# Kernel optimization log

Measured on AMD Instinct MI355X. Metric: run time of the kernel, lower is better.

Reference implementation:

```python
import jax, jax.numpy as jnp
import numpy as np

NUM_HEADS = 12
HEAD_SIZE = 64
HIDDEN = NUM_HEADS * HEAD_SIZE  # 768
ONE_SIDED_WINDOW = 256          # attention_window 512 // 2
NEG = -10000.0


def setup_inputs() -> dict:
    key = jax.random.key(0)
    ks = jax.random.split(key, 16)
    B, W, E, H = 1, 2048, 128, HIDDEN
    std = 0.02
    def lin(kw, kb):
        return (jax.random.normal(kw, (H, H), jnp.float32) * std,
                jax.random.normal(kb, (H,), jnp.float32) * std)
    q_w, q_b = lin(ks[0], ks[1])
    k_w, k_b = lin(ks[2], ks[3])
    v_w, v_b = lin(ks[4], ks[5])
    w2e_w, w2e_b = lin(ks[6], ks[7])
    e2w_w, e2w_b = lin(ks[8], ks[9])
    e2e_w, e2e_b = lin(ks[10], ks[11])
    return {
        "word_hidden_states": jax.random.normal(ks[12], (B, W, H), jnp.float32),
        "entity_hidden_states": jax.random.normal(ks[13], (B, E, H), jnp.float32),
        "attention_mask": jnp.zeros((B, 1, 1, W + E), jnp.float32),
        "q_w": q_w, "q_b": q_b, "k_w": k_w, "k_b": k_b, "v_w": v_w, "v_b": v_b,
        "w2e_w": w2e_w, "w2e_b": w2e_b, "e2w_w": e2w_w, "e2w_b": e2w_b,
        "e2e_w": e2e_w, "e2e_b": e2e_b,
    }


def reference(word_hidden_states, entity_hidden_states, attention_mask,
              q_w, q_b, k_w, k_b, v_w, v_b,
              w2e_w, w2e_b, e2w_w, e2w_b, e2e_w, e2e_b):
    B, W, H = word_hidden_states.shape
    E = entity_hidden_states.shape[1]
    S = W + E

    def heads(x):  # [B, L, H] -> [B, nh, L, hd]
        return x.reshape(B, -1, NUM_HEADS, HEAD_SIZE).transpose(0, 2, 1, 3)

    concat = jnp.concatenate([word_hidden_states, entity_hidden_states], axis=1)
    k = heads(concat @ k_w + k_b)          # [B, nh, S, hd]
    v = heads(concat @ v_w + v_b)
    q_w2w = heads(word_hidden_states @ q_w + q_b)
    q_w2e = heads(word_hidden_states @ w2e_w + w2e_b)
    q_e2w = heads(entity_hidden_states @ e2w_w + e2w_b)
    q_e2e = heads(entity_hidden_states @ e2e_w + e2e_b)

    k_word, k_ent = k[:, :, :W], k[:, :, W:]

    # --- w2w: Longformer sliding-window QK^T, then _conversion to a dense
    # [B, nh, W, W] matrix with out-of-band entries set to -10000. ---
    w2w = jnp.einsum('bhid,bhjd->bhij', q_w2w, k_word)  # [B, nh, W, W]
    idx = jnp.arange(W)
    in_band = jnp.abs(idx[:, None] - idx[None, :]) <= ONE_SIDED_WINDOW  # [W, W]
    # diagonal mask: float_mask[j] (-10000 where attention_mask != 0) added
    # within the band (broadcast over heads / query positions)
    mask_words = attention_mask[:, 0, 0, :W]                # [B, W]
    float_mask = jnp.where(mask_words != 0.0, NEG, 0.0)     # [B, W]
    w2w = w2w + float_mask[:, None, None, :]
    # _conversion: out-of-band -> -10000; also exact zeros -> -10000 (source quirk)
    w2w = jnp.where(in_band[None, None] & (w2w != 0.0), w2w, NEG)

    # --- entity-aware dense blocks ---
    w2e = jnp.einsum('bhid,bhjd->bhij', q_w2e, k_ent)    # [B, nh, W, E]
    e2w = jnp.einsum('bhid,bhjd->bhij', q_e2w, k_word)   # [B, nh, E, W]
    e2e = jnp.einsum('bhid,bhjd->bhij', q_e2e, k_ent)    # [B, nh, E, E]

    word_scores = jnp.concatenate([w2w, w2e], axis=3)    # [B, nh, W, S]
    ent_scores = jnp.concatenate([e2w, e2e], axis=3)     # [B, nh, E, S]
    scores = jnp.concatenate([word_scores, ent_scores], axis=2)  # [B, nh, S, S]

    scores = scores / jnp.sqrt(jnp.float32(HEAD_SIZE)) + attention_mask
    probs = jax.nn.softmax(scores, axis=-1)

    ctx = jnp.einsum('bhij,bhjd->bhid', probs, v)        # [B, nh, S, hd]
    ctx = ctx.transpose(0, 2, 1, 3).reshape(B, S, H)
    return ctx[:, :W, :], ctx[:, W:, :]
```

## Files before the change

### kernel.cpp

```cpp
#include <hip/hip_runtime.h>

typedef __bf16 bf16x8 __attribute__((ext_vector_type(8)));
typedef unsigned short u16x8 __attribute__((ext_vector_type(8)));
typedef u16x8 u16x8_a __attribute__((may_alias));
typedef unsigned int u32x2 __attribute__((ext_vector_type(2)));
typedef u32x2 u32x2_a __attribute__((may_alias));
typedef unsigned int u32x4 __attribute__((ext_vector_type(4)));
typedef u32x4 u32x4_a __attribute__((may_alias));
typedef float f32x4 __attribute__((ext_vector_type(4)));

#define LOG2E 1.4426950408889634f
#define NEGV  -10000.0f

__device__ __forceinline__ unsigned int cvtpk(float lo, float hi){
  unsigned int r;
  asm("v_cvt_pk_bf16_f32 %0, %1, %2" : "=v"(r) : "v"(lo), "v"(hi));
  return r;
}
__device__ __forceinline__ bf16x8 ldb(const unsigned short* p){
  return __builtin_bit_cast(bf16x8, *(const u16x8_a*)p);
}
__device__ __forceinline__ void gload16(const unsigned short* g, unsigned short* l){
  __builtin_amdgcn_global_load_lds(
    (const __attribute__((address_space(1))) void*)g,
    (__attribute__((address_space(3))) void*)l, 16, 0, 0);
}

__global__ __launch_bounds__(256) void prep(
    const float* __restrict__ w0, const float* __restrict__ w1,
    const float* __restrict__ w2, const float* __restrict__ w3,
    const float* __restrict__ w4, const float* __restrict__ w5,
    const float* __restrict__ word, const float* __restrict__ ent,
    const float* __restrict__ am,
    unsigned short* __restrict__ outT, unsigned short* __restrict__ Abf,
    float* __restrict__ amT, float* __restrict__ negT)
{
  int z = blockIdx.z, tid = threadIdx.x;
  if (z == 6){
    size_t id = (size_t)blockIdx.y*24 + blockIdx.x;
    size_t e = (id*256 + tid)*8;
    const size_t WE = (size_t)2048*768;
    const float* s = (e < WE) ? (word + e) : (ent + (e - WE));
    float4 a = *(const float4*)s;
    float4 b = *(const float4*)(s+4);
    u32x4 v = {cvtpk(a.x,a.y), cvtpk(a.z,a.w), cvtpk(b.x,b.y), cvtpk(b.z,b.w)};
    *(u32x4_a*)(Abf + e) = v;
    return;
  }
  if (z == 7){
    if (blockIdx.y != 0 || blockIdx.x >= 9) return;
    int j = blockIdx.x*256 + tid;
    if (j < 2176){
      float a = am[j];
      amT[j]  = a * LOG2E;
      negT[j] = (a != 0.f) ? NEGV : 0.f;
    }
    return;
  }
  if (blockIdx.y >= 24) return;
  const float* src;
  switch (z){
    case 0: src = w0; break; case 1: src = w1; break; case 2: src = w2; break;
    case 3: src = w3; break; case 4: src = w4; break; default: src = w5; break;
  }
  unsigned short* dst = outT + (size_t)z * 589824;
  __shared__ float tile[32][33];
  int tx = tid & 31, ty = tid >> 5;
  int x0 = blockIdx.x*32, y0 = blockIdx.y*32;
  #pragma unroll
  for (int i=0;i<32;i+=8) tile[ty+i][tx] = src[(size_t)(y0+ty+i)*768 + x0+tx];
  __syncthreads();
  #pragma unroll
  for (int i=0;i<32;i+=16){
    unsigned int u = cvtpk(tile[tx][ty+i], tile[tx][ty+i+8]);
    dst[(size_t)(x0+ty+i)*768 + y0+tx]   = (unsigned short)u;
    dst[(size_t)(x0+ty+i+8)*768 + y0+tx] = (unsigned short)(u>>16);
  }
}

__global__ __launch_bounds__(256) void gemm_proj(
    const unsigned short* __restrict__ Abf,
    const unsigned short* __restrict__ wT,
    const float* __restrict__ bK, const float* __restrict__ bV,
    const float* __restrict__ bQ, const float* __restrict__ bWE,
    const float* __restrict__ bEW, const float* __restrict__ bEE,
    unsigned short* __restrict__ oK, unsigned short* __restrict__ VbT,
    unsigned short* __restrict__ oQ, unsigned short* __restrict__ oWE,
    unsigned short* __restrict__ oEW, unsigned short* __restrict__ oEE)
{
  int mt = blockIdx.x, ntile = blockIdx.y;
  int g, mg;
  if      (mt < 17){ g=0; mg=mt;    }
  else if (mt < 34){ g=1; mg=mt-17; }
  else if (mt < 50){ g=2; mg=mt-34; }
  else if (mt < 66){ g=3; mg=mt-50; }
  else if (mt < 67){ g=4; mg=0;     }
  else             { g=5; mg=0;     }
  int m0 = mg*128;
  const unsigned short* A = Abf + (size_t)((g>=4 ? 2048 : 0) + m0)*768;
  const unsigned short* B = wT + (size_t)g*589824;
  const float* bias; unsigned short* out;
  switch (g){
    case 0: bias=bK;  out=oK;  break;
    case 1: bias=bV;  out=0;   break;
    case 2: bias=bQ;  out=oQ;  break;
    case 3: bias=bWE; out=oWE; break;
    case 4: bias=bEW; out=oEW; break;
    default:bias=bEE; out=oEE; break;
  }
  int n0 = ntile*128;

  __shared__ __align__(16) unsigned short a_s[128*32];
  __shared__ __align__(16) unsigned short b_s[128*32];

  int tid  = threadIdx.x;
  int w    = tid>>6, lane = tid&63, quad = lane>>4, lr = lane&15;
  int wm   = (w&1)*64, wn = (w>>1)*64;

  f32x4 acc[4][4];
  #pragma unroll
  for (int i=0;i<4;i++) for (int j=0;j<4;j++) for (int r=0;r<4;r++) acc[i][j][r]=0.f;

  int srow = lane>>2;
  int scol = (lane&3)*8;
  const unsigned short* gA0 = A + (size_t)(w*32 + srow)*768 + scol;
  const unsigned short* gA1 = gA0 + (size_t)16*768;
  const unsigned short* gB0 = B + (size_t)(n0 + w*32 + srow)*768 + scol;
  const unsigned short* gB1 = gB0 + (size_t)16*768;
  unsigned short* lA0 = a_s + w*32*32;
  unsigned short* lA1 = lA0 + 16*32;
  unsigned short* lB0 = b_s + w*32*32;
  unsigned short* lB1 = lB0 + 16*32;

  for (int k0=0; k0<768; k0+=32){
    __syncthreads();
    gload16(gA0 + k0, lA0);
    gload16(gA1 + k0, lA1);
    gload16(gB0 + k0, lB0);
    gload16(gB1 + k0, lB1);
    __syncthreads();
    bf16x8 af[4], bfr[4];
    #pragma unroll
    for (int i=0;i<4;i++) af[i]  = ldb(a_s + (wm+i*16+lr)*32 + quad*8);
    #pragma unroll
    for (int j=0;j<4;j++) bfr[j] = ldb(b_s + (wn+j*16+lr)*32 + quad*8);
    #pragma unroll
    for (int i=0;i<4;i++)
      #pragma unroll
      for (int j=0;j<4;j++)
        acc[i][j] = __builtin_amdgcn_mfma_f32_16x16x32_bf16(af[i], bfr[j], acc[i][j], 0,0,0);
  }
  if (g == 1){
    #pragma unroll
    for (int j=0;j<4;j++){
      int col = n0 + wn + j*16 + lr;
      float bb = bias[col];
      #pragma unroll
      for (int i=0;i<4;i++){
        int rowb = m0 + wm + i*16 + quad*4;
        u32x2 uv = {cvtpk(acc[i][j][0]+bb, acc[i][j][1]+bb),
                    cvtpk(acc[i][j][2]+bb, acc[i][j][3]+bb)};
        *(u32x2_a*)(VbT + (size_t)col*2176 + rowb) = uv;
      }
    }
  } else {
    out += (size_t)m0*768;
    #pragma unroll
    for (int j=0;j<4;j++){
      int col = n0 + wn + j*16 + lr;
      float bb = bias[col];
      #pragma unroll
      for (int i=0;i<4;i++){
        int rowb = wm + i*16 + quad*4;
        unsigned int u01 = cvtpk(acc[i][j][0]+bb, acc[i][j][1]+bb);
        unsigned int u23 = cvtpk(acc[i][j][2]+bb, acc[i][j][3]+bb);
        out[(size_t)(rowb+0)*768 + col] = (unsigned short)u01;
        out[(size_t)(rowb+1)*768 + col] = (unsigned short)(u01>>16);
        out[(size_t)(rowb+2)*768 + col] = (unsigned short)u23;
        out[(size_t)(rowb+3)*768 + col] = (unsigned short)(u23>>16);
      }
    }
  }
}

__global__ __launch_bounds__(256) void attn_split(
  const unsigned short* __restrict__ Kb,  const unsigned short* __restrict__ VbT,
  const unsigned short* __restrict__ Qw,  const unsigned short* __restrict__ Qwe,
  const unsigned short* __restrict__ Qew, const unsigned short* __restrict__ Qee,
  const float* __restrict__ amT, const float* __restrict__ negT,
  float* __restrict__ outw, float* __restrict__ pO, float* __restrict__ pML)
{
  int lin = blockIdx.x + 80*blockIdx.y;
  int wid = (lin & 7)*120 + (lin >> 3);
  int bx = wid % 80;
  int h  = wid / 80;

  int tid = threadIdx.x, w = tid>>6, lane = tid&63, quad = lane>>4, lr = lane&15;
  bool isword = bx < 64;
  int qrb, kh, nsplit, eg=0, ehalf=0;
  const unsigned short *Qa, *Qb;
  if (isword){ qrb = bx*32 + (w>>1)*16; kh = w&1; nsplit = 2; Qa=Qw;  Qb=Qwe; }
  else       { int e = bx-64; eg = e>>1; ehalf = e&1;
               qrb = eg*16;             kh = w;   nsplit = 4; Qa=Qew; Qb=Qee; }
  int hofs = h*64;

  __shared__ __align__(16) unsigned int shb[4*64*21];
  unsigned int* p32w = shb + w*(16*44);

  const unsigned short* qr = Qa + (size_t)(qrb+lr)*768 + hofs + quad*8;
  bf16x8 qa0 = ldb(qr), qa1 = ldb(qr + 32);
  qr = Qb + (size_t)(qrb+lr)*768 + hofs + quad*8;
  bf16x8 qb0 = ldb(qr), qb1 = ldb(qr + 32);

  u16x8 onesu;
  #pragma unroll
  for (int i=0;i<8;i++) onesu[i] = 0x3F80;
  bf16x8 onesf = __builtin_bit_cast(bf16x8, onesu);

  float m = -1e30f;
  f32x4 o[4], l4;
  #pragma unroll
  for (int r=0;r<4;r++) l4[r] = 0.f;
  #pragma unroll
  for (int n2=0;n2<4;n2++) for (int r=0;r<4;r++) o[n2][r] = 0.f;

  int lo, nw, start, end, step;
  if (isword){
    lo = qrb - 256; if (lo < 0) lo = 0; lo &= ~31;
    int hi = qrb + 272; if (hi > 2048) hi = 2048; hi = (hi + 31) & ~31;
    nw = (hi - lo) >> 5;
    start = kh; end = nw + 4; step = 2;
  } else {
    lo = 0; nw = 64;
    start = ehalf*34 + kh; end = ehalf*34 + 34; step = 4;
  }
  int iq = qrb + lr;

  for (int c = start; c < end; c += 2*step){
    int c2r = c + step;
    bool ph = (c2r >= end);
    int c2 = ph ? c : c2r;

    bool entp1 = c  >= nw;  int j1 = entp1 ? (2048 + (c -nw)*32) : (lo + c *32);
    bool entp2 = c2 >= nw;  int j2 = entp2 ? (2048 + (c2-nw)*32) : (lo + c2*32);

    const unsigned short* kp1 = Kb + (size_t)(j1+lr)*768 + hofs + quad*8;
    bf16x8 kA0 = ldb(kp1),          kA1 = ldb(kp1 + 32);
    bf16x8 kA2 = ldb(kp1 + 16*768), kA3 = ldb(kp1 + 16*768 + 32);
    const unsigned short* kp2 = Kb + (size_t)(j2+lr)*768 + hofs + quad*8;
    bf16x8 kB0 = ldb(kp2),          kB1 = ldb(kp2 + 32);
    bf16x8 kB2 = ldb(kp2 + 16*768), kB3 = ldb(kp2 + 16*768 + 32);
    const unsigned short* vp1 = VbT + (size_t)(hofs + lr)*2176 + j1 + quad*8;
    bf16x8 v10 = ldb(vp1), v11 = ldb(vp1 + 16*2176), v12 = ldb(vp1 + 32*2176), v13 = ldb(vp1 + 48*2176);
    float4 aA0 = *(const float4*)(amT + j1 + quad*4);
    float4 aA1 = *(const float4*)(amT + j1 + 16 + quad*4);
    float4 aB0 = *(const float4*)(amT + j2 + quad*4);
    float4 aB1 = *(const float4*)(amT + j2 + 16 + quad*4);
    float4 nA0 = *(const float4*)(negT + j1 + quad*4);
    float4 nA1 = *(const float4*)(negT + j1 + 16 + quad*4);
    float4 nB0 = *(const float4*)(negT + j2 + quad*4);
    float4 nB1 = *(const float4*)(negT + j2 + 16 + quad*4);

    bf16x8 qf10 = entp1 ? qb0 : qa0, qf11 = entp1 ? qb1 : qa1;
    bf16x8 qf20 = entp2 ? qb0 : qa0, qf21 = entp2 ? qb1 : qa1;

    f32x4 sA0 = {0.f,0.f,0.f,0.f}, sA1 = {0.f,0.f,0.f,0.f};
    f32x4 sB0 = {0.f,0.f,0.f,0.f}, sB1 = {0.f,0.f,0.f,0.f};
    __builtin_amdgcn_s_setprio(1);
    sA0 = __builtin_amdgcn_mfma_f32_16x16x32_bf16(kA0, qf10, sA0, 0,0,0);
    sA0 = __builtin_amdgcn_mfma_f32_16x16x32_bf16(kA1, qf11, sA0, 0,0,0);
    sA1 = __builtin_amdgcn_mfma_f32_16x16x32_bf16(kA2, qf10, sA1, 0,0,0);
    sA1 = __builtin_amdgcn_mfma_f32_16x16x32_bf16(kA3, qf11, sA1, 0,0,0);
    sB0 = __builtin_amdgcn_mfma_f32_16x16x32_bf16(kB0, qf20, sB0, 0,0,0);
    sB0 = __builtin_amdgcn_mfma_f32_16x16x32_bf16(kB1, qf21, sB0, 0,0,0);
    sB1 = __builtin_amdgcn_mfma_f32_16x16x32_bf16(kB2, qf20, sB1, 0,0,0);
    sB1 = __builtin_amdgcn_mfma_f32_16x16x32_bf16(kB3, qf21, sB1, 0,0,0);
    __builtin_amdgcn_s_setprio(0);

    float scA0[4], scA1[4], scB0[4], scB1[4];
    bool wb1 = isword && !entp1;
    bool wb2 = isword && !entp2;
    #pragma unroll
    for (int r=0;r<4;r++){
      { float sv = sA0[r];
        if (wb1){ sv += nA0[r];
          int j = j1 + quad*4 + r;
          bool ok = ((unsigned)(iq - j + 256) <= 512u) && (sv != 0.f);
          sv = ok ? sv : NEGV; }
        scA0[r] = sv * (LOG2E*0.125f) + aA0[r]; }
      { float sv = sA1[r];
        if (wb1){ sv += nA1[r];
          int j = j1 + 16 + quad*4 + r;
          bool ok = ((unsigned)(iq - j + 256) <= 512u) && (sv != 0.f);
          sv = ok ? sv : NEGV; }
        scA1[r] = sv * (LOG2E*0.125f) + aA1[r]; }
      { float sv = sB0[r];
        if (wb2){ sv += nB0[r];
          int j = j2 + quad*4 + r;
          bool ok = ((unsigned)(iq - j + 256) <= 512u) && (sv != 0.f);
          sv = ok ? sv : NEGV; }
        scB0[r] = sv * (LOG2E*0.125f) + aB0[r]; }
      { float sv = sB1[r];
        if (wb2){ sv += nB1[r];
          int j = j2 + 16 + quad*4 + r;
          bool ok = ((unsigned)(iq - j + 256) <= 512u) && (sv != 0.f);
          sv = ok ? sv : NEGV; }
        scB1[r] = sv * (LOG2E*0.125f) + aB1[r]; }
    }
    if (ph){
      #pragma unroll
      for (int r=0;r<4;r++){ scB0[r] = -1e30f; scB1[r] = -1e30f; }
    }

    float mx = fmaxf(
      fmaxf(fmaxf(fmaxf(scA0[0],scA0[1]), fmaxf(scA0[2],scA0[3])),
            fmaxf(fmaxf(scA1[0],scA1[1]), fmaxf(scA1[2],scA1[3]))),
      fmaxf(fmaxf(fmaxf(scB0[0],scB0[1]), fmaxf(scB0[2],scB0[3])),
            fmaxf(fmaxf(scB1[0],scB1[1]), fmaxf(scB1[2],scB1[3]))));
    mx = fmaxf(mx, __shfl_xor(mx, 16));
    mx = fmaxf(mx, __shfl_xor(mx, 32));

    float mn;
    if (__all(mx <= m)){
      mn = m;
    } else {
      mn = fmaxf(m, mx);
      float alpha = exp2f(m - mn);
      m = mn;
      #pragma unroll
      for (int r=0;r<4;r++) l4[r] *= alpha;
      #pragma unroll
      for (int n2=0;n2<4;n2++)
        #pragma unroll
        for (int r=0;r<4;r++) o[n2][r] *= alpha;
    }

    unsigned int xA0 = cvtpk(exp2f(scA0[0]-mn), exp2f(scA0[1]-mn));
    unsigned int xA1 = cvtpk(exp2f(scA0[2]-mn), exp2f(scA0[3]-mn));
    unsigned int xA2 = cvtpk(exp2f(scA1[0]-mn), exp2f(scA1[1]-mn));
    unsigned int xA3 = cvtpk(exp2f(scA1[2]-mn), exp2f(scA1[3]-mn));
    unsigned int xB0 = cvtpk(exp2f(scB0[0]-mn), exp2f(scB0[1]-mn));
    unsigned int xB1 = cvtpk(exp2f(scB0[2]-mn), exp2f(scB0[3]-mn));
    unsigned int xB2 = cvtpk(exp2f(scB1[0]-mn), exp2f(scB1[1]-mn));
    unsigned int xB3 = cvtpk(exp2f(scB1[2]-mn), exp2f(scB1[3]-mn));

    unsigned int* row = p32w + lr*44;
    u32x2 wv0 = {xA0, xA1};
    u32x2 wv1 = {xA2, xA3};
    u32x2 wv2 = {xB0, xB1};
    u32x2 wv3 = {xB2, xB3};
    *(u32x2_a*)(row + quad*2)      = wv0;
    *(u32x2_a*)(row + 8  + quad*2) = wv1;
    *(u32x2_a*)(row + 16 + quad*2) = wv2;
    *(u32x2_a*)(row + 24 + quad*2) = wv3;
    bf16x8 pf1 = ldb((const unsigned short*)(p32w + lr*44 + quad*4));
    bf16x8 pf2 = ldb((const unsigned short*)(p32w + lr*44 + 16 + quad*4));

    __builtin_amdgcn_s_setprio(1);
    o[0] = __builtin_amdgcn_mfma_f32_16x16x32_bf16(v10, pf1, o[0], 0,0,0);
    o[1] = __builtin_amdgcn_mfma_f32_16x16x32_bf16(v11, pf1, o[1], 0,0,0);
    o[2] = __builtin_amdgcn_mfma_f32_16x16x32_bf16(v12, pf1, o[2], 0,0,0);
    o[3] = __builtin_amdgcn_mfma_f32_16x16x32_bf16(v13, pf1, o[3], 0,0,0);
    l4   = __builtin_amdgcn_mfma_f32_16x16x32_bf16(onesf, pf1, l4, 0,0,0);
    __builtin_amdgcn_s_setprio(0);

    const unsigned short* vp2 = VbT + (size_t)(hofs + lr)*2176 + j2 + quad*8;
    bf16x8 v20 = ldb(vp2), v21 = ldb(vp2 + 16*2176), v22 = ldb(vp2 + 32*2176), v23 = ldb(vp2 + 48*2176);

    __builtin_amdgcn_s_setprio(1);
    o[0] = __builtin_amdgcn_mfma_f32_16x16x32_bf16(v20, pf2, o[0], 0,0,0);
    o[1] = __builtin_amdgcn_mfma_f32_16x16x32_bf16(v21, pf2, o[1], 0,0,0);
    o[2] = __builtin_amdgcn_mfma_f32_16x16x32_bf16(v22, pf2, o[2], 0,0,0);
    o[3] = __builtin_amdgcn_mfma_f32_16x16x32_bf16(v23, pf2, o[3], 0,0,0);
    l4   = __builtin_amdgcn_mfma_f32_16x16x32_bf16(onesf, pf2, l4, 0,0,0);
    __builtin_amdgcn_s_setprio(0);
  }

  float lsc = l4[0];
  __syncthreads();
  {
    float* my = (float*)shb + ((size_t)(w*64 + lane))*21;
    my[0] = m; my[1] = lsc;
    #pragma unroll
    for (int n2=0;n2<4;n2++)
      #pragma unroll
      for (int r=0;r<4;r++) my[2+n2*4+r] = o[n2][r];
  }
  __syncthreads();
  if (kh == 0){
    for (int p=1; p<nsplit; p++){
      const float* pr = (float*)shb + ((size_t)((w+p)*64 + lane))*21;
      float m2 = pr[0], l2 = pr[1];
      float M  = fmaxf(m, m2);
      float e1 = exp2f(m-M), e2 = exp2f(m2-M);
      m = M;
      lsc = lsc*e1 + l2*e2;
      #pragma unroll
      for (int n2=0;n2<4;n2++)
        #pragma unroll
        for (int r=0;r<4;r++)
          o[n2][r] = o[n2][r]*e1 + pr[2+n2*4+r]*e2;
    }
    if (isword){
      float rinv = 1.f / lsc;
      #pragma unroll
      for (int n2=0;n2<4;n2++){
        float4 sv;
        sv.x = o[n2][0]*rinv; sv.y = o[n2][1]*rinv;
        sv.z = o[n2][2]*rinv; sv.w = o[n2][3]*rinv;
        *(float4*)(outw + (size_t)(qrb+lr)*768 + hofs + n2*16 + quad*4) = sv;
      }
    } else {
      int idx = (eg*12 + h)*2 + ehalf;
      float* po = pO + (size_t)idx*1024;
      #pragma unroll
      for (int n2=0;n2<4;n2++){
        float4 sv;
        sv.x = o[n2][0]; sv.y = o[n2][1]; sv.z = o[n2][2]; sv.w = o[n2][3];
        *(float4*)(po + lr*64 + n2*16 + quad*4) = sv;
      }
      if (quad == 0){
        float* pml = pML + (size_t)idx*32;
        pml[lr*2]     = m;
        pml[lr*2 + 1] = lsc;
      }
    }
  }
}

__global__ __launch_bounds__(256) void merge_ent(
    const float* __restrict__ pO, const float* __restrict__ pML,
    float* __restrict__ oute)
{
  int b = blockIdx.x;
  int g = b/12, h = b%12;
  int tid = threadIdx.x;
  int row = tid>>4, cg = tid&15;
  int i0 = b*2, i1 = b*2+1;
  float m0 = pML[(size_t)i0*32 + row*2], l0 = pML[(size_t)i0*32 + row*2 + 1];
  float m1 = pML[(size_t)i1*32 + row*2], l1 = pML[(size_t)i1*32 + row*2 + 1];
  float M  = fmaxf(m0, m1);
  float e0 = exp2f(m0-M), e1 = exp2f(m1-M);
  float rl = 1.f/(l0*e0 + l1*e1);
  float4 a = *(const float4*)(pO + (size_t)i0*1024 + row*64 + cg*4);
  float4 c = *(const float4*)(pO + (size_t)i1*1024 + row*64 + cg*4);
  float4 o;
  o.x = (a.x*e0 + c.x*e1)*rl;
  o.y = (a.y*e0 + c.y*e1)*rl;
  o.z = (a.z*e0 + c.z*e1)*rl;
  o.w = (a.w*e0 + c.w*e1)*rl;
  *(float4*)(oute + (size_t)(g*16+row)*768 + h*64 + cg*4) = o;
}

extern "C" void kernel_launch(void* const* d_in, const int* in_sizes, int n_in,
                              void* d_out, int out_size, void* d_ws, size_t ws_size,
                              hipStream_t stream) {
  const float* word  = (const float*)d_in[0];
  const float* ent   = (const float*)d_in[1];
  const float* am    = (const float*)d_in[2];
  const float* q_w   = (const float*)d_in[3];
  const float* q_b   = (const float*)d_in[4];
  const float* k_w   = (const float*)d_in[5];
  const float* k_b   = (const float*)d_in[6];
  const float* v_w   = (const float*)d_in[7];
  const float* v_b   = (const float*)d_in[8];
  const float* w2e_w = (const float*)d_in[9];
  const float* w2e_b = (const float*)d_in[10];
  const float* e2w_w = (const float*)d_in[11];
  const float* e2w_b = (const float*)d_in[12];
  const float* e2e_w = (const float*)d_in[13];
  const float* e2e_b = (const float*)d_in[14];

  unsigned short* ws  = (unsigned short*)d_ws;
  unsigned short* wT  = ws;
  unsigned short* Kb  = wT  + (size_t)6*589824;
  unsigned short* Tb  = Kb  + (size_t)2176*768;
  unsigned short* Qw  = Tb  + (size_t)2176*768;
  unsigned short* Qwe = Qw  + (size_t)2048*768;
  unsigned short* Qew = Qwe + (size_t)2048*768;
  unsigned short* Qee = Qew + (size_t)128*768;
  unsigned short* VbT = Qee + (size_t)128*768;
  unsigned short* Abf = VbT + (size_t)768*2176;

  float* amT  = (float*)Tb;
  float* negT = amT + 2176;

  float* pO  = (float*)wT;
  float* pML = pO + (size_t)192*1024;

  float* outw = (float*)d_out;
  float* oute = outw + (size_t)2048*768;

  hipLaunchKernelGGL(prep, dim3(24,34,8), dim3(256), 0, stream,
                     k_w, v_w, q_w, w2e_w, e2w_w, e2e_w, word, ent, am,
                     wT, Abf, amT, negT);
  hipLaunchKernelGGL(gemm_proj, dim3(68,6), dim3(256), 0, stream,
                     Abf, wT, k_b, v_b, q_b, w2e_b, e2w_b, e2e_b,
                     Kb, VbT, Qw, Qwe, Qew, Qee);
  hipLaunchKernelGGL(attn_split, dim3(80,12), dim3(256), 0, stream,
                     Kb, VbT, Qw, Qwe, Qew, Qee, amT, negT, outw, pO, pML);
  hipLaunchKernelGGL(merge_ent, dim3(96), dim3(256), 0, stream,
                     pO, pML, oute);
}
```

Before: 169.4 us.

## Switch attention to 32x32x16 MFMA tiles with register-shuffled P fragments

Rewrites the attention kernel to compute each 32-query by 32-key tile with 32x32x16 bf16 MFMAs instead of pairs of 16x16x32 ops. The probability fragment is built by cross-half lane shuffles instead of a round trip through shared memory. The row sum is accumulated with adds instead of a ones-matrix MFMA. Each of the four waves now handles a strided slice of the key chunks, and a four-way shared-memory merge combines them. Entity blocks are regrouped into 32-row groups with four key splits, and merge_ent is updated to combine four partials; the larger accumulators raise register pressure.

Result: faster. 152.9 us (-9.8%).

```diff
diff --git a/kernel.cpp b/kernel.cpp
--- a/kernel.cpp
+++ b/kernel.cpp
@@ -8,6 +8,7 @@
 typedef unsigned int u32x4 __attribute__((ext_vector_type(4)));
 typedef u32x4 u32x4_a __attribute__((may_alias));
 typedef float f32x4 __attribute__((ext_vector_type(4)));
+typedef float f32x16 __attribute__((ext_vector_type(16)));
 
 #define LOG2E 1.4426950408889634f
 #define NEGV  -10000.0f
@@ -19,6 +20,10 @@
 }
 __device__ __forceinline__ bf16x8 ldb(const unsigned short* p){
   return __builtin_bit_cast(bf16x8, *(const u16x8_a*)p);
+}
+__device__ __forceinline__ bf16x8 mkfrag(unsigned a, unsigned b, unsigned c, unsigned d){
+  u32x4 v = {a,b,c,d};
+  return __builtin_bit_cast(bf16x8, v);
 }
 __device__ __forceinline__ void gload16(const unsigned short* g, unsigned short* l){
   __builtin_amdgcn_global_load_lds(
@@ -195,129 +200,102 @@
   int bx = wid % 80;
   int h  = wid / 80;
 
-  int tid = threadIdx.x, w = tid>>6, lane = tid&63, quad = lane>>4, lr = lane&15;
+  int tid = threadIdx.x, w = tid>>6, lane = tid&63;
+  int l31 = lane & 31, hi = lane >> 5;
+  int hi8 = hi*8, hi4 = hi*4;
   bool isword = bx < 64;
-  int qrb, kh, nsplit, eg=0, ehalf=0;
+  int qrb, eg=0, eq=0;
   const unsigned short *Qa, *Qb;
-  if (isword){ qrb = bx*32 + (w>>1)*16; kh = w&1; nsplit = 2; Qa=Qw;  Qb=Qwe; }
-  else       { int e = bx-64; eg = e>>1; ehalf = e&1;
-               qrb = eg*16;             kh = w;   nsplit = 4; Qa=Qew; Qb=Qee; }
+  if (isword){ qrb = bx*32; Qa=Qw;  Qb=Qwe; }
+  else       { int e = bx-64; eg = e>>2; eq = e&3; qrb = eg*32; Qa=Qew; Qb=Qee; }
   int hofs = h*64;
 
-  __shared__ __align__(16) unsigned int shb[4*64*21];
-  unsigned int* p32w = shb + w*(16*44);
-
-  const unsigned short* qr = Qa + (size_t)(qrb+lr)*768 + hofs + quad*8;
-  bf16x8 qa0 = ldb(qr), qa1 = ldb(qr + 32);
-  qr = Qb + (size_t)(qrb+lr)*768 + hofs + quad*8;
-  bf16x8 qb0 = ldb(qr), qb1 = ldb(qr + 32);
-
-  u16x8 onesu;
-  #pragma unroll
-  for (int i=0;i<8;i++) onesu[i] = 0x3F80;
-  bf16x8 onesf = __builtin_bit_cast(bf16x8, onesu);
-
-  float m = -1e30f;
-  f32x4 o[4], l4;
-  #pragma unroll
-  for (int r=0;r<4;r++) l4[r] = 0.f;
-  #pragma unroll
-  for (int n2=0;n2<4;n2++) for (int r=0;r<4;r++) o[n2][r] = 0.f;
-
-  int lo, nw, start, end, step;
+  __shared__ float part[4][64][35];
+
+  const unsigned short* qr = Qa + (size_t)(qrb+l31)*768 + hofs + hi8;
+  bf16x8 qa0 = ldb(qr), qa1 = ldb(qr+16), qa2 = ldb(qr+32), qa3 = ldb(qr+48);
+  qr = Qb + (size_t)(qrb+l31)*768 + hofs + hi8;
+  bf16x8 qb0 = ldb(qr), qb1 = ldb(qr+16), qb2 = ldb(qr+32), qb3 = ldb(qr+48);
+
+  float m = -1e30f, l = 0.f;
+  f32x16 o0, o1;
+  #pragma unroll
+  for (int r=0;r<16;r++){ o0[r] = 0.f; o1[r] = 0.f; }
+
+  int lo, nw, start, end;
   if (isword){
-    lo = qrb - 256; if (lo < 0) lo = 0; lo &= ~31;
-    int hi = qrb + 272; if (hi > 2048) hi = 2048; hi = (hi + 31) & ~31;
-    nw = (hi - lo) >> 5;
-    start = kh; end = nw + 4; step = 2;
+    lo = qrb - 256; if (lo < 0) lo = 0;
+    int hiq = qrb + 288; if (hiq > 2048) hiq = 2048;
+    nw = (hiq - lo) >> 5;
+    start = w; end = nw + 4;
   } else {
     lo = 0; nw = 64;
-    start = ehalf*34 + kh; end = ehalf*34 + 34; step = 4;
-  }
-  int iq = qrb + lr;
-
-  for (int c = start; c < end; c += 2*step){
-    int c2r = c + step;
-    bool ph = (c2r >= end);
-    int c2 = ph ? c : c2r;
-
-    bool entp1 = c  >= nw;  int j1 = entp1 ? (2048 + (c -nw)*32) : (lo + c *32);
-    bool entp2 = c2 >= nw;  int j2 = entp2 ? (2048 + (c2-nw)*32) : (lo + c2*32);
-
-    const unsigned short* kp1 = Kb + (size_t)(j1+lr)*768 + hofs + quad*8;
-    bf16x8 kA0 = ldb(kp1),          kA1 = ldb(kp1 + 32);
-    bf16x8 kA2 = ldb(kp1 + 16*768), kA3 = ldb(kp1 + 16*768 + 32);
-    const unsigned short* kp2 = Kb + (size_t)(j2+lr)*768 + hofs + quad*8;
-    bf16x8 kB0 = ldb(kp2),          kB1 = ldb(kp2 + 32);
-    bf16x8 kB2 = ldb(kp2 + 16*768), kB3 = ldb(kp2 + 16*768 + 32);
-    const unsigned short* vp1 = VbT + (size_t)(hofs + lr)*2176 + j1 + quad*8;
-    bf16x8 v10 = ldb(vp1), v11 = ldb(vp1 + 16*2176), v12 = ldb(vp1 + 32*2176), v13 = ldb(vp1 + 48*2176);
-    float4 aA0 = *(const float4*)(amT + j1 + quad*4);
-    float4 aA1 = *(const float4*)(amT + j1 + 16 + quad*4);
-    float4 aB0 = *(const float4*)(amT + j2 + quad*4);
-    float4 aB1 = *(const float4*)(amT + j2 + 16 + quad*4);
-    float4 nA0 = *(const float4*)(negT + j1 + quad*4);
-    float4 nA1 = *(const float4*)(negT + j1 + 16 + quad*4);
-    float4 nB0 = *(const float4*)(negT + j2 + quad*4);
-    float4 nB1 = *(const float4*)(negT + j2 + 16 + quad*4);
-
-    bf16x8 qf10 = entp1 ? qb0 : qa0, qf11 = entp1 ? qb1 : qa1;
-    bf16x8 qf20 = entp2 ? qb0 : qa0, qf21 = entp2 ? qb1 : qa1;
-
-    f32x4 sA0 = {0.f,0.f,0.f,0.f}, sA1 = {0.f,0.f,0.f,0.f};
-    f32x4 sB0 = {0.f,0.f,0.f,0.f}, sB1 = {0.f,0.f,0.f,0.f};
+    start = eq*17 + w; end = eq*17 + 17;
+  }
+  int iq = qrb + l31;
+
+  for (int c = start; c < end; c += 4){
+    bool entp = c >= nw;
+    int j0 = entp ? (2048 + (c-nw)*32) : (lo + c*32);
+
+    const unsigned short* kp = Kb + (size_t)(j0+l31)*768 + hofs + hi8;
+    bf16x8 ka0 = ldb(kp), ka1 = ldb(kp+16), ka2 = ldb(kp+32), ka3 = ldb(kp+48);
+    const unsigned short* vp = VbT + (size_t)(hofs + l31)*2176 + j0 + hi8;
+    bf16x8 va00 = ldb(vp),           va01 = ldb(vp + 16);
+    bf16x8 va10 = ldb(vp + 32*2176), va11 = ldb(vp + 32*2176 + 16);
+    float4 aT0 = *(const float4*)(amT + j0 + hi4);
+    float4 aT1 = *(const float4*)(amT + j0 + 8  + hi4);
+    float4 aT2 = *(const float4*)(amT + j0 + 16 + hi4);
+    float4 aT3 = *(const float4*)(amT + j0 + 24 + hi4);
+
+    bf16x8 qf0 = entp ? qb0 : qa0, qf1 = entp ? qb1 : qa1;
+    bf16x8 qf2 = entp ? qb2 : qa2, qf3 = entp ? qb3 : qa3;
+
+    f32x16 s;
+    #pragma unroll
+    for (int r=0;r<16;r++) s[r] = 0.f;
     __builtin_amdgcn_s_setprio(1);
-    sA0 = __builtin_amdgcn_mfma_f32_16x16x32_bf16(kA0, qf10, sA0, 0,0,0);
-    sA0 = __builtin_amdgcn_mfma_f32_16x16x32_bf16(kA1, qf11, sA0, 0,0,0);
-    sA1 = __builtin_amdgcn_mfma_f32_16x16x32_bf16(kA2, qf10, sA1, 0,0,0);
-    sA1 = __builtin_amdgcn_mfma_f32_16x16x32_bf16(kA3, qf11, sA1, 0,0,0);
-    sB0 = __builtin_amdgcn_mfma_f32_16x16x32_bf16(kB0, qf20, sB0, 0,0,0);
-    sB0 = __builtin_amdgcn_mfma_f32_16x16x32_bf16(kB1, qf21, sB0, 0,0,0);
-    sB1 = __builtin_amdgcn_mfma_f32_16x16x32_bf16(kB2, qf20, sB1, 0,0,0);
-    sB1 = __builtin_amdgcn_mfma_f32_16x16x32_bf16(kB3, qf21, sB1, 0,0,0);
+    s = __builtin_amdgcn_mfma_f32_32x32x16_bf16(ka0, qf0, s, 0,0,0);
+    s = __builtin_amdgcn_mfma_f32_32x32x16_bf16(ka1, qf1, s, 0,0,0);
+    s = __builtin_amdgcn_mfma_f32_32x32x16_bf16(ka2, qf2, s, 0,0,0);
+    s = __builtin_amdgcn_mfma_f32_32x32x16_bf16(ka3, qf3, s, 0,0,0);
     __builtin_amdgcn_s_setprio(0);
 
-    float scA0[4], scA1[4], scB0[4], scB1[4];
-    bool wb1 = isword && !entp1;
-    bool wb2 = isword && !entp2;
-    #pragma unroll
-    for (int r=0;r<4;r++){
-      { float sv = sA0[r];
-        if (wb1){ sv += nA0[r];
-          int j = j1 + quad*4 + r;
-          bool ok = ((unsigned)(iq - j + 256) <= 512u) && (sv != 0.f);
-          sv = ok ? sv : NEGV; }
-        scA0[r] = sv * (LOG2E*0.125f) + aA0[r]; }
-      { float sv = sA1[r];
-        if (wb1){ sv += nA1[r];
-          int j = j1 + 16 + quad*4 + r;
-          bool ok = ((unsigned)(iq - j + 256) <= 512u) && (sv != 0.f);
-          sv = ok ? sv : NEGV; }
-        scA1[r] = sv * (LOG2E*0.125f) + aA1[r]; }
-      { float sv = sB0[r];
-        if (wb2){ sv += nB0[r];
-          int j = j2 + quad*4 + r;
-          bool ok = ((unsigned)(iq - j + 256) <= 512u) && (sv != 0.f);
-          sv = ok ? sv : NEGV; }
-        scB0[r] = sv * (LOG2E*0.125f) + aB0[r]; }
-      { float sv = sB1[r];
-        if (wb2){ sv += nB1[r];
-          int j = j2 + 16 + quad*4 + r;
-          bool ok = ((unsigned)(iq - j + 256) <= 512u) && (sv != 0.f);
-          sv = ok ? sv : NEGV; }
-        scB1[r] = sv * (LOG2E*0.125f) + aB1[r]; }
-    }
-    if (ph){
-      #pragma unroll
-      for (int r=0;r<4;r++){ scB0[r] = -1e30f; scB1[r] = -1e30f; }
-    }
-
-    float mx = fmaxf(
-      fmaxf(fmaxf(fmaxf(scA0[0],scA0[1]), fmaxf(scA0[2],scA0[3])),
-            fmaxf(fmaxf(scA1[0],scA1[1]), fmaxf(scA1[2],scA1[3]))),
-      fmaxf(fmaxf(fmaxf(scB0[0],scB0[1]), fmaxf(scB0[2],scB0[3])),
-            fmaxf(fmaxf(scB1[0],scB1[1]), fmaxf(scB1[2],scB1[3]))));
-    mx = fmaxf(mx, __shfl_xor(mx, 16));
+    float sc[16];
+    if (isword && !entp){
+      float4 nT0 = *(const float4*)(negT + j0 + hi4);
+      float4 nT1 = *(const float4*)(negT + j0 + 8  + hi4);
+      float4 nT2 = *(const float4*)(negT + j0 + 16 + hi4);
+      float4 nT3 = *(const float4*)(negT + j0 + 24 + hi4);
+      int djb = iq + 256 - (j0 + hi4);
+      #pragma unroll
+      for (int e=0;e<4;e++){
+        { float sv = s[e]    + nT0[e];
+          bool ok = ((unsigned)(djb - e)      <= 512u) && (sv != 0.f);
+          sc[e]    = (ok ? sv : NEGV) * (LOG2E*0.125f) + aT0[e]; }
+        { float sv = s[4+e]  + nT1[e];
+          bool ok = ((unsigned)(djb - 8 - e)  <= 512u) && (sv != 0.f);
+          sc[4+e]  = (ok ? sv : NEGV) * (LOG2E*0.125f) + aT1[e]; }
+        { float sv = s[8+e]  + nT2[e];
+          bool ok = ((unsigned)(djb - 16 - e) <= 512u) && (sv != 0.f);
+          sc[8+e]  = (ok ? sv : NEGV) * (LOG2E*0.125f) + aT2[e]; }
+        { float sv = s[12+e] + nT3[e];
+          bool ok = ((unsigned)(djb - 24 - e) <= 512u) && (sv != 0.f);
+          sc[12+e] = (ok ? sv : NEGV) * (LOG2E*0.125f) + aT3[e]; }
+      }
+    } else {
+      #pragma unroll
+      for (int e=0;e<4;e++){
+        sc[e]    = s[e]    * (LOG2E*0.125f) + aT0[e];
+        sc[4+e]  = s[4+e]  * (LOG2E*0.125f) + aT1[e];
+        sc[8+e]  = s[8+e]  * (LOG2E*0.125f) + aT2[e];
+        sc[12+e] = s[12+e] * (LOG2E*0.125f) + aT3[e];
+      }
+    }
+
+    float mx = sc[0];
+    #pragma unroll
+    for (int r=1;r<16;r++) mx = fmaxf(mx, sc[r]);
     mx = fmaxf(mx, __shfl_xor(mx, 32));
 
     float mn;
@@ -327,103 +305,91 @@
       mn = fmaxf(m, mx);
       float alpha = exp2f(m - mn);
       m = mn;
-      #pragma unroll
-      for (int r=0;r<4;r++) l4[r] *= alpha;
-      #pragma unroll
-      for (int n2=0;n2<4;n2++)
-        #pragma unroll
-        for (int r=0;r<4;r++) o[n2][r] *= alpha;
-    }
-
-    unsigned int xA0 = cvtpk(exp2f(scA0[0]-mn), exp2f(scA0[1]-mn));
-    unsigned int xA1 = cvtpk(exp2f(scA0[2]-mn), exp2f(scA0[3]-mn));
-    unsigned int xA2 = cvtpk(exp2f(scA1[0]-mn), exp2f(scA1[1]-mn));
-    unsigned int xA3 = cvtpk(exp2f(scA1[2]-mn), exp2f(scA1[3]-mn));
-    unsigned int xB0 = cvtpk(exp2f(scB0[0]-mn), exp2f(scB0[1]-mn));
-    unsigned int xB1 = cvtpk(exp2f(scB0[2]-mn), exp2f(scB0[3]-mn));
-    unsigned int xB2 = cvtpk(exp2f(scB1[0]-mn), exp2f(scB1[1]-mn));
-    unsigned int xB3 = cvtpk(exp2f(scB1[2]-mn), exp2f(scB1[3]-mn));
-
-    unsigned int* row = p32w + lr*44;
-    u32x2 wv0 = {xA0, xA1};
-    u32x2 wv1 = {xA2, xA3};
-    u32x2 wv2 = {xB0, xB1};
-    u32x2 wv3 = {xB2, xB3};
-    *(u32x2_a*)(row + quad*2)      = wv0;
-    *(u32x2_a*)(row + 8  + quad*2) = wv1;
-    *(u32x2_a*)(row + 16 + quad*2) = wv2;
-    *(u32x2_a*)(row + 24 + quad*2) = wv3;
-    bf16x8 pf1 = ldb((const unsigned short*)(p32w + lr*44 + quad*4));
-    bf16x8 pf2 = ldb((const unsigned short*)(p32w + lr*44 + 16 + quad*4));
+      l *= alpha;
+      #pragma unroll
+      for (int r=0;r<16;r++){ o0[r] *= alpha; o1[r] *= alpha; }
+    }
+
+    float p[16];
+    #pragma unroll
+    for (int r=0;r<16;r++) p[r] = exp2f(sc[r]-mn);
+
+    float rs = ((p[0]+p[1])+(p[2]+p[3])) + ((p[4]+p[5])+(p[6]+p[7]))
+             + ((p[8]+p[9])+(p[10]+p[11])) + ((p[12]+p[13])+(p[14]+p[15]));
+    rs += __shfl_xor(rs, 32);
+    l += rs;
+
+    unsigned pk0 = cvtpk(p[0], p[1]),  pk1 = cvtpk(p[2], p[3]);
+    unsigned pk2 = cvtpk(p[4], p[5]),  pk3 = cvtpk(p[6], p[7]);
+    unsigned pk4 = cvtpk(p[8], p[9]),  pk5 = cvtpk(p[10], p[11]);
+    unsigned pk6 = cvtpk(p[12], p[13]),pk7 = cvtpk(p[14], p[15]);
+
+    bool hib = hi != 0;
+    unsigned t0 = hib ? pk0 : pk2;
+    unsigned t1 = hib ? pk1 : pk3;
+    unsigned t2 = hib ? pk4 : pk6;
+    unsigned t3 = hib ? pk5 : pk7;
+    unsigned r0 = (unsigned)__shfl_xor((int)t0, 32);
+    unsigned r1 = (unsigned)__shfl_xor((int)t1, 32);
+    unsigned r2 = (unsigned)__shfl_xor((int)t2, 32);
+    unsigned r3 = (unsigned)__shfl_xor((int)t3, 32);
+    bf16x8 pf1 = hib ? mkfrag(r0, r1, pk2, pk3) : mkfrag(pk0, pk1, r0, r1);
+    bf16x8 pf2 = hib ? mkfrag(r2, r3, pk6, pk7) : mkfrag(pk4, pk5, r2, r3);
 
     __builtin_amdgcn_s_setprio(1);
-    o[0] = __builtin_amdgcn_mfma_f32_16x16x32_bf16(v10, pf1, o[0], 0,0,0);
-    o[1] = __builtin_amdgcn_mfma_f32_16x16x32_bf16(v11, pf1, o[1], 0,0,0);
-    o[2] = __builtin_amdgcn_mfma_f32_16x16x32_bf16(v12, pf1, o[2], 0,0,0);
-    o[3] = __builtin_amdgcn_mfma_f32_16x16x32_bf16(v13, pf1, o[3], 0,0,0);
-    l4   = __builtin_amdgcn_mfma_f32_16x16x32_bf16(onesf, pf1, l4, 0,0,0);
+    o0 = __builtin_amdgcn_mfma_f32_32x32x16_bf16(va00, pf1, o0, 0,0,0);
+    o0 = __builtin_amdgcn_mfma_f32_32x32x16_bf16(va01, pf2, o0, 0,0,0);
+    o1 = __builtin_amdgcn_mfma_f32_32x32x16_bf16(va10, pf1, o1, 0,0,0);
+    o1 = __builtin_amdgcn_mfma_f32_32x32x16_bf16(va11, pf2, o1, 0,0,0);
     __builtin_amdgcn_s_setprio(0);
-
-    const unsigned short* vp2 = VbT + (size_t)(hofs + lr)*2176 + j2 + quad*8;
-    bf16x8 v20 = ldb(vp2), v21 = ldb(vp2 + 16*2176), v22 = ldb(vp2 + 32*2176), v23 = ldb(vp2 + 48*2176);
-
-    __builtin_amdgcn_s_setprio(1);
-    o[0] = __builtin_amdgcn_mfma_f32_16x16x32_bf16(v20, pf2, o[0], 0,0,0);
-    o[1] = __builtin_amdgcn_mfma_f32_16x16x32_bf16(v21, pf2, o[1], 0,0,0);
-    o[2] = __builtin_amdgcn_mfma_f32_16x16x32_bf16(v22, pf2, o[2], 0,0,0);
-    o[3] = __builtin_amdgcn_mfma_f32_16x16x32_bf16(v23, pf2, o[3], 0,0,0);
-    l4   = __builtin_amdgcn_mfma_f32_16x16x32_bf16(onesf, pf2, l4, 0,0,0);
-    __builtin_amdgcn_s_setprio(0);
-  }
-
-  float lsc = l4[0];
+  }
+
+  {
+    float* my = &part[w][lane][0];
+    my[0] = m; my[1] = l;
+    #pragma unroll
+    for (int r=0;r<16;r++){ my[2+r] = o0[r]; my[18+r] = o1[r]; }
+  }
   __syncthreads();
-  {
-    float* my = (float*)shb + ((size_t)(w*64 + lane))*21;
-    my[0] = m; my[1] = lsc;
-    #pragma unroll
-    for (int n2=0;n2<4;n2++)
-      #pragma unroll
-      for (int r=0;r<4;r++) my[2+n2*4+r] = o[n2][r];
-  }
-  __syncthreads();
-  if (kh == 0){
-    for (int p=1; p<nsplit; p++){
-      const float* pr = (float*)shb + ((size_t)((w+p)*64 + lane))*21;
-      float m2 = pr[0], l2 = pr[1];
-      float M  = fmaxf(m, m2);
-      float e1 = exp2f(m-M), e2 = exp2f(m2-M);
-      m = M;
-      lsc = lsc*e1 + l2*e2;
-      #pragma unroll
-      for (int n2=0;n2<4;n2++)
-        #pragma unroll
-        for (int r=0;r<4;r++)
-          o[n2][r] = o[n2][r]*e1 + pr[2+n2*4+r]*e2;
-    }
-    if (isword){
-      float rinv = 1.f / lsc;
-      #pragma unroll
-      for (int n2=0;n2<4;n2++){
-        float4 sv;
-        sv.x = o[n2][0]*rinv; sv.y = o[n2][1]*rinv;
-        sv.z = o[n2][2]*rinv; sv.w = o[n2][3]*rinv;
-        *(float4*)(outw + (size_t)(qrb+lr)*768 + hofs + n2*16 + quad*4) = sv;
-      }
-    } else {
-      int idx = (eg*12 + h)*2 + ehalf;
-      float* po = pO + (size_t)idx*1024;
-      #pragma unroll
-      for (int n2=0;n2<4;n2++){
-        float4 sv;
-        sv.x = o[n2][0]; sv.y = o[n2][1]; sv.z = o[n2][2]; sv.w = o[n2][3];
-        *(float4*)(po + lr*64 + n2*16 + quad*4) = sv;
-      }
-      if (quad == 0){
-        float* pml = pML + (size_t)idx*32;
-        pml[lr*2]     = m;
-        pml[lr*2 + 1] = lsc;
-      }
+
+  float mm[4], ll[4], e4[4];
+  #pragma unroll
+  for (int p=0;p<4;p++){ mm[p] = part[p][lane][0]; ll[p] = part[p][lane][1]; }
+  float M = fmaxf(fmaxf(mm[0],mm[1]), fmaxf(mm[2],mm[3]));
+  #pragma unroll
+  for (int p=0;p<4;p++) e4[p] = exp2f(mm[p]-M);
+  float L = ll[0]*e4[0] + ll[1]*e4[1] + ll[2]*e4[2] + ll[3]*e4[3];
+
+  float mo0[4], mo1[4];
+  #pragma unroll
+  for (int k=0;k<4;k++){
+    float a0 = 0.f, a1 = 0.f;
+    #pragma unroll
+    for (int p=0;p<4;p++){
+      a0 += part[p][lane][2  + w*4 + k] * e4[p];
+      a1 += part[p][lane][18 + w*4 + k] * e4[p];
+    }
+    mo0[k] = a0; mo1[k] = a1;
+  }
+
+  if (isword){
+    float rinv = 1.f / L;
+    float4 s0 = {mo0[0]*rinv, mo0[1]*rinv, mo0[2]*rinv, mo0[3]*rinv};
+    float4 s1 = {mo1[0]*rinv, mo1[1]*rinv, mo1[2]*rinv, mo1[3]*rinv};
+    float* ob = outw + (size_t)(qrb+l31)*768 + hofs + w*8 + hi4;
+    *(float4*)(ob)      = s0;
+    *(float4*)(ob + 32) = s1;
+  } else {
+    int idx = (eg*4 + eq)*12 + h;
+    float* po = pO + (size_t)idx*2048 + l31*64 + w*8 + hi4;
+    float4 s0 = {mo0[0], mo0[1], mo0[2], mo0[3]};
+    float4 s1 = {mo1[0], mo1[1], mo1[2], mo1[3]};
+    *(float4*)(po)      = s0;
+    *(float4*)(po + 32) = s1;
+    if (w == 0 && lane < 32){
+      float* pml = pML + (size_t)idx*64;
+      pml[lane*2]     = M;
+      pml[lane*2 + 1] = L;
     }
   }
 }
@@ -433,23 +399,36 @@
     float* __restrict__ oute)
 {
   int b = blockIdx.x;
-  int g = b/12, h = b%12;
+  int eg = b/12, h = b%12;
   int tid = threadIdx.x;
-  int row = tid>>4, cg = tid&15;
-  int i0 = b*2, i1 = b*2+1;
-  float m0 = pML[(size_t)i0*32 + row*2], l0 = pML[(size_t)i0*32 + row*2 + 1];
-  float m1 = pML[(size_t)i1*32 + row*2], l1 = pML[(size_t)i1*32 + row*2 + 1];
-  float M  = fmaxf(m0, m1);
-  float e0 = exp2f(m0-M), e1 = exp2f(m1-M);
-  float rl = 1.f/(l0*e0 + l1*e1);
-  float4 a = *(const float4*)(pO + (size_t)i0*1024 + row*64 + cg*4);
-  float4 c = *(const float4*)(pO + (size_t)i1*1024 + row*64 + cg*4);
-  float4 o;
-  o.x = (a.x*e0 + c.x*e1)*rl;
-  o.y = (a.y*e0 + c.y*e1)*rl;
-  o.z = (a.z*e0 + c.z*e1)*rl;
-  o.w = (a.w*e0 + c.w*e1)*rl;
-  *(float4*)(oute + (size_t)(g*16+row)*768 + h*64 + cg*4) = o;
+  int row = tid>>3, cg = (tid&7)*8;
+  float mq[4], lq[4];
+  #pragma unroll
+  for (int q=0;q<4;q++){
+    int idx = (eg*4 + q)*12 + h;
+    mq[q] = pML[(size_t)idx*64 + row*2];
+    lq[q] = pML[(size_t)idx*64 + row*2 + 1];
+  }
+  float M = fmaxf(fmaxf(mq[0],mq[1]), fmaxf(mq[2],mq[3]));
+  float L = 0.f, eqv[4];
+  #pragma unroll
+  for (int q=0;q<4;q++){ eqv[q] = exp2f(mq[q]-M); L += lq[q]*eqv[q]; }
+  float rl = 1.f/L;
+  float4 a0 = {0,0,0,0}, a1 = {0,0,0,0};
+  #pragma unroll
+  for (int q=0;q<4;q++){
+    int idx = (eg*4 + q)*12 + h;
+    const float* src = pO + (size_t)idx*2048 + row*64 + cg;
+    float4 x = *(const float4*)(src);
+    float4 y = *(const float4*)(src + 4);
+    a0.x += x.x*eqv[q]; a0.y += x.y*eqv[q]; a0.z += x.z*eqv[q]; a0.w += x.w*eqv[q];
+    a1.x += y.x*eqv[q]; a1.y += y.y*eqv[q]; a1.z += y.z*eqv[q]; a1.w += y.w*eqv[q];
+  }
+  a0.x*=rl; a0.y*=rl; a0.z*=rl; a0.w*=rl;
+  a1.x*=rl; a1.y*=rl; a1.z*=rl; a1.w*=rl;
+  float* dst = oute + (size_t)(eg*32+row)*768 + h*64 + cg;
+  *(float4*)(dst)   = a0;
+  *(float4*)(dst+4) = a1;
 }
 
 extern "C" void kernel_launch(void* const* d_in, const int* in_sizes, int n_in,
@@ -486,7 +465,7 @@
   float* negT = amT + 2176;
 
   float* pO  = (float*)wT;
-  float* pML = pO + (size_t)192*1024;
+  float* pML = pO + (size_t)192*2048;
 
   float* outw = (float*)d_out;
   float* oute = outw + (size_t)2048*768;
@@ -499,6 +478,6 @@
                      Kb, VbT, Qw, Qwe, Qew, Qee);
   hipLaunchKernelGGL(attn_split, dim3(80,12), dim3(256), 0, stream,
                      Kb, VbT, Qw, Qwe, Qew, Qee, amT, negT, outw, pO, pML);
-  hipLaunchKernelGGL(merge_ent, dim3(96), dim3(256), 0, stream,
+  hipLaunchKernelGGL(merge_ent, dim3(48), dim3(256), 0, stream,
                      pO, pML, oute);
 }
```
